# Performance work log

Measured on AMD Instinct MI355X. Metric: run time of the kernel, lower is better.

## Reference

```python
import jax, jax.numpy as jnp
import numpy as np

NUM_LAYERS = 3
N = 4096
DIM = 512
TOPK = 8
BIG = 1.0e9
EPS_COS = 1e-8
EPS_NORM = 1e-12
BN_EPS = 1e-5
LAM_K = 64.0
LAM_Z = 16.0
SIGMA_INTRA = 0.99
ALPHA = np.linspace(1.0, 1.2, NUM_LAYERS)
BETA = np.linspace(0.0, 0.0, NUM_LAYERS)


def setup_inputs() -> dict:
    key = jax.random.key(0)
    ks = jax.random.split(key, 6)
    feats = jax.random.normal(ks[0], (NUM_LAYERS, N, DIM), dtype=jnp.float32)
    labels = jax.random.randint(ks[1], (N,), 0, 64, dtype=jnp.int64)
    fc1_w = jax.random.normal(ks[2], (NUM_LAYERS, DIM, DIM), dtype=jnp.float32) * (1.0 / np.sqrt(DIM))
    fc2_w = jax.random.normal(ks[3], (NUM_LAYERS, DIM, DIM), dtype=jnp.float32) * (1.0 / np.sqrt(DIM))
    bn_gamma = jnp.ones((NUM_LAYERS, DIM), dtype=jnp.float32)
    bn_beta = jnp.zeros((NUM_LAYERS, DIM), dtype=jnp.float32)
    proj_w = jax.random.normal(ks[4], (768, DIM), dtype=jnp.float32) * (1.0 / np.sqrt(DIM))
    return {"feats": feats, "labels": labels, "fc1_w": fc1_w, "fc2_w": fc2_w,
            "bn_gamma": bn_gamma, "bn_beta": bn_beta, "proj_w": proj_w}


def _l2norm(x, axis=-1):
    return x / jnp.maximum(jnp.linalg.norm(x, axis=axis, keepdims=True), EPS_NORM)


def _pairwise_cosine(G):
    Gn = _l2norm(G)
    sim = Gn @ Gn.T
    return jnp.clip(sim, -1.0 + EPS_COS, 1.0 - EPS_COS)


def _knn_mask(sim, base_mask, topk):
    n = sim.shape[0]
    masked = (sim - BIG * jnp.eye(n, dtype=sim.dtype)) * base_mask - (1.0 - base_mask) * BIG
    k = min(topk, max(n - 1, 1))
    idx = jax.lax.top_k(masked, k)[1]  # [N, k]
    st = jnp.zeros_like(sim).at[jnp.arange(n)[:, None], idx].set(1.0)
    return jnp.maximum(st, st.T)


def _build_intra_inter(sim, labels, topk):
    same = (labels[None, :] == labels[:, None]).astype(sim.dtype)
    diff = 1.0 - same
    m_intra = _knn_mask(sim, same, topk)
    m_inter = _knn_mask(sim, diff, topk)
    sim_intra = jnp.maximum(sim * m_intra, 0.0)
    sim_inter = jnp.maximum(sim * m_inter, 0.0)
    return sim_intra, sim_inter


def _normalize_sym(sim_graph, eps=1e-8):
    d = jnp.maximum(sim_graph.sum(axis=1), eps)
    dinv = d ** -0.5
    return dinv[:, None] * sim_graph * dinv[None, :]  # == diag(dinv) @ S @ diag(dinv)


def _diffusion(K, t_diff=1):
    out = K
    for _ in range(max(t_diff - 1, 0)):
        out = out @ K
    return out


def _bn_train(x, gamma, beta):
    m = x.mean(axis=0)
    v = x.var(axis=0)  # biased, as torch BN training
    return (x - m) / jnp.sqrt(v + BN_EPS) * gamma + beta


def _gam(S, G, w1, w2, gamma, beta):
    Z = S @ (G @ w1.T)
    Z = jax.nn.relu(_bn_train(Z, gamma, beta))
    Z = S @ (Z @ w2.T)
    return Z + G


def reference(feats, labels, fc1_w, fc2_w, bn_gamma, bn_beta, proj_w):
    n = feats.shape[1]
    eye = jnp.eye(n, dtype=feats.dtype)
    same = (labels[None, :] == labels[:, None]).astype(feats.dtype)

    K_list, Z_list = [], []
    for i in range(NUM_LAYERS):
        G = feats[i]
        sim = _pairwise_cosine(G)
        sim_intra, sim_inter = _build_intra_inter(sim, labels, TOPK)
        sim_graph = float(ALPHA[i]) * sim_intra + float(BETA[i]) * sim_inter + 1e-6 * eye
        S = _normalize_sym(sim_graph)
        K = _diffusion(S, t_diff=1)
        Z = _gam(S, G, fc1_w[i], fc2_w[i], bn_gamma[i], bn_beta[i])
        K_list.append(K)
        Z_list.append(Z)

    loss_K = jnp.zeros((), dtype=feats.dtype)
    loss_Z = jnp.zeros((), dtype=feats.dtype)
    for i in range(1, NUM_LAYERS):
        K_tgt = jax.lax.stop_gradient(K_list[i])
        loss_K = loss_K + jnp.mean((K_list[i - 1] - K_tgt) ** 2)
        Zp = _l2norm(Z_list[i - 1] @ proj_w.T)
        Zc = _l2norm(Z_list[i] @ proj_w.T)
        loss_Z = loss_Z + jnp.mean((Zp - jax.lax.stop_gradient(Zc)) ** 2)

    K_idea = _diffusion(same * SIGMA_INTRA, t_diff=1)
    loss_idea = jnp.mean((K_list[-1] - K_idea) ** 2)
    return LAM_K * loss_K + LAM_Z * loss_Z + loss_idea
```

## Files before the change

kernel.cpp:

```cpp
#include <hip/hip_runtime.h>
#include <math.h>
#include <stdint.h>

#define NROWS 4096
#define DIM   512
#define NCLS  64
#define CAP   128
#define PD    768
#define NL    3

typedef __attribute__((ext_vector_type(8))) short short8v;
typedef __attribute__((ext_vector_type(4))) float f32x4;

__device__ __forceinline__ unsigned short f2bf(float f) {
  unsigned u = __float_as_uint(f);
  unsigned r = (u + 0x7FFF + ((u >> 16) & 1)) >> 16;
  return (unsigned short)r;
}

__device__ __forceinline__ void gload_lds16(const void* g, void* l) {
  auto* lp = reinterpret_cast<__attribute__((address_space(3))) unsigned int*>(
      reinterpret_cast<uintptr_t>(l));
  const auto* gp = reinterpret_cast<const __attribute__((address_space(1))) unsigned int*>(
      reinterpret_cast<uintptr_t>(g));
  __builtin_amdgcn_global_load_lds(gp, lp, 16, 0, 0);
}

__device__ __forceinline__ float waveReduce(float v) {
#pragma unroll
  for (int o = 32; o > 0; o >>= 1) v += __shfl_down(v, o);
  return v;
}

__device__ __forceinline__ float blockReduce(float v) {
  __shared__ float sh[4];
  int lane = threadIdx.x & 63, wv = threadIdx.x >> 6;
  v = waveReduce(v);
  if (lane == 0) sh[wv] = v;
  __syncthreads();
  float t = 0.f;
  if (threadIdx.x == 0) {
    int nw = (blockDim.x + 63) >> 6;
    for (int i = 0; i < nw; ++i) t += sh[i];
  }
  return t;
}

__global__ __launch_bounds__(256) void k_hist(const int* __restrict__ labels, int* __restrict__ chunkCnt) {
  __shared__ int h[NCLS];
  int t = threadIdx.x;
  if (t < NCLS) h[t] = 0;
  __syncthreads();
  atomicAdd(&h[labels[blockIdx.x * 256 + t]], 1);
  __syncthreads();
  if (t < NCLS) chunkCnt[blockIdx.x * NCLS + t] = h[t];
}

__global__ void k_scan(const int* __restrict__ chunkCnt, int* __restrict__ cnt,
                       int* __restrict__ off, int* __restrict__ chunkBase, float* __restrict__ acc) {
  __shared__ int sc[NCLS];
  int c = threadIdx.x;
  if (c < 8) acc[c] = 0.f;
  int tot = 0;
  for (int b = 0; b < 16; ++b) tot += chunkCnt[b * NCLS + c];
  cnt[c] = tot;
  sc[c] = tot;
  __syncthreads();
  if (c == 0) {
    int s = 0;
    for (int i = 0; i < NCLS; ++i) { int tv = sc[i]; sc[i] = s; s += tv; }
  }
  __syncthreads();
  int run = sc[c];
  off[c] = run;
  for (int b = 0; b < 16; ++b) { chunkBase[b * NCLS + c] = run; run += chunkCnt[b * NCLS + c]; }
  if (c == 0) off[NCLS] = NROWS;
}

__global__ __launch_bounds__(256) void k_scatter(const int* __restrict__ labels, const int* __restrict__ chunkBase,
                                                 int* __restrict__ perm, int* __restrict__ clsp) {
  __shared__ int lab[256];
  int t = threadIdx.x;
  int r = blockIdx.x * 256 + t;
  int c = labels[r];
  lab[t] = c;
  __syncthreads();
  int rank = 0;
  for (int j = 0; j < t; ++j) rank += (lab[j] == c);
  int pos = chunkBase[blockIdx.x * NCLS + c] + rank;
  perm[pos] = r;
  clsp[pos] = c;
}

__global__ __launch_bounds__(128) void k_prep(const float* __restrict__ feats, const int* __restrict__ perm,
                                              unsigned short* __restrict__ Gpb, float* __restrict__ invn) {
  __shared__ float red[2];
  int l = blockIdx.y;
  const float* G = feats + (size_t)l * NROWS * DIM;
  unsigned short* Gp = Gpb + (size_t)l * NROWS * DIM;
  int row = blockIdx.x, t = threadIdx.x;
  const float4* src = (const float4*)(G + (size_t)perm[row] * DIM);
  float4 v = src[t];
  ushort4 b;
  b.x = f2bf(v.x); b.y = f2bf(v.y); b.z = f2bf(v.z); b.w = f2bf(v.w);
  *(ushort4*)(Gp + (size_t)row * DIM + t * 4) = b;
  float ss = v.x * v.x + v.y * v.y + v.z * v.z + v.w * v.w;
  ss = waveReduce(ss);
  if ((t & 63) == 0) red[t >> 6] = ss;
  __syncthreads();
  if (t == 0) invn[l * NROWS + row] = 1.f / fmaxf(sqrtf(red[0] + red[1]), 1e-12f);
}

__global__ __launch_bounds__(256) void k_tobf16all(const float4* __restrict__ fc1, const float4* __restrict__ fc2,
                                                   const float4* __restrict__ proj,
                                                   ushort4* __restrict__ w1, ushort4* __restrict__ w2,
                                                   ushort4* __restrict__ pj) {
  const int nW = NL * DIM * DIM / 4;
  const int nP = PD * DIM / 4;
  int i = blockIdx.x * 256 + threadIdx.x;
  const float4* src; ushort4* dst; int k;
  if (i < nW) { src = fc1; dst = w1; k = i; }
  else if (i < 2 * nW) { src = fc2; dst = w2; k = i - nW; }
  else if (i < 2 * nW + nP) { src = proj; dst = pj; k = i - 2 * nW; }
  else return;
  float4 v = src[k];
  ushort4 o;
  o.x = f2bf(v.x); o.y = f2bf(v.y); o.z = f2bf(v.z); o.w = f2bf(v.w);
  dst[k] = o;
}

__global__ __launch_bounds__(256) void k_sim(const unsigned short* __restrict__ Gpb,
                                             const float* __restrict__ invn,
                                             const int* __restrict__ cnt, const int* __restrict__ off,
                                             float* __restrict__ sim) {
  int l = blockIdx.z;
  const unsigned short* Gp = Gpb + (size_t)l * NROWS * DIM;
  const float* inv = invn + (size_t)l * NROWS;
  float* sm = sim + (size_t)l * NCLS * CAP * CAP;
  int c = blockIdx.y;
  int n = min(cnt[c], CAP);
  int ti = blockIdx.x >> 2, tj = blockIdx.x & 3;
  if (ti * 32 >= n || tj * 32 >= n) return;
  int base = off[c];
  __shared__ short As[32][40];
  __shared__ short Bs[32][40];
  const int t = threadIdx.x;
  const int lane = t & 63, wv = t >> 6;
  const int qi = wv >> 1, qj = wv & 1;
  const int fr = lane & 15, kg = lane >> 4;
  const int half = t >> 7, tt = t & 127;
  const int srow = tt >> 2, scol = (tt & 3) * 8;
  int gr = (half ? tj : ti) * 32 + srow;
  const unsigned short* ps = Gp + (size_t)(base + min(gr, n - 1)) * DIM + scol;
  short* dst = half ? &Bs[srow][scol] : &As[srow][scol];
  f32x4 acc = {};
  for (int k0 = 0; k0 < DIM; k0 += 32) {
    short8v v = *(const short8v*)(ps + k0);
    __syncthreads();
    *(short8v*)dst = v;
    __syncthreads();
    short8v af = *(const short8v*)&As[qi * 16 + fr][kg * 8];
    short8v bf = *(const short8v*)&Bs[qj * 16 + fr][kg * 8];
    acc = __builtin_amdgcn_mfma_f32_16x16x32_bf16(af, bf, acc, 0, 0, 0);
  }
  int gj = tj * 32 + qj * 16 + fr;
  int r0 = ti * 32 + qi * 16 + kg * 4;
  if (gj < n) {
    float sj = inv[base + gj];
#pragma unroll
    for (int r = 0; r < 4; ++r) {
      int gi = r0 + r;
      if (gi < n) {
        float v = acc[r] * inv[base + gi] * sj;
        v = fminf(fmaxf(v, -1.0f + 1e-8f), 1.0f - 1e-8f);
        sm[((size_t)c * CAP + gi) * CAP + gj] = v;
      }
    }
  }
}

__global__ __launch_bounds__(64) void k_topk(const float* __restrict__ sim, const int* __restrict__ cnt,
                                             const int* __restrict__ off, const int* __restrict__ clsp,
                                             int* __restrict__ t8) {
  int l = blockIdx.y;
  const float* sm = sim + (size_t)l * NCLS * CAP * CAP;
  int* t8l = t8 + (size_t)l * NROWS * 8;
  int pr = blockIdx.x * 64 + threadIdx.x;
  if (pr >= NROWS) return;
  int c = clsp[pr];
  int n = min(cnt[c], CAP);
  int loc = pr - off[c];
  const float* row = sm + ((size_t)c * CAP + loc) * CAP;
  float bv[8]; int bi[8];
#pragma unroll
  for (int q = 0; q < 8; ++q) { bv[q] = -3e38f; bi[q] = -1; }
  for (int j = 0; j < n; ++j) {
    if (j == loc) continue;
    float v = row[j];
    if (v > bv[7]) {
      bv[7] = v; bi[7] = j;
#pragma unroll
      for (int q = 7; q > 0; --q) {
        if (bv[q] > bv[q - 1]) {
          float tv = bv[q]; bv[q] = bv[q - 1]; bv[q - 1] = tv;
          int tq = bi[q]; bi[q] = bi[q - 1]; bi[q - 1] = tq;
        }
      }
    }
  }
#pragma unroll
  for (int q = 0; q < 8; ++q) t8l[pr * 8 + q] = bi[q];
}

__global__ __launch_bounds__(256) void k_buildS1(const float* __restrict__ sim, const int* __restrict__ cnt,
                                                 const int* __restrict__ off, const int* __restrict__ t8,
                                                 float* __restrict__ S, float* __restrict__ dinv) {
  int l = blockIdx.z;
  float alpha = 1.0f + 0.1f * l;
  const float* sm = sim + (size_t)l * NCLS * CAP * CAP;
  float* Sl = S + (size_t)l * NCLS * CAP * CAP;
  const int* t8l = t8 + (size_t)l * NROWS * 8;
  float* dv = dinv + (size_t)l * NCLS * CAP;
  int c = blockIdx.x;
  int n = min(cnt[c], CAP);
  int i0 = blockIdx.y * 32;
  if (i0 >= n) return;
  int base = off[c];
  __shared__ int sh8[CAP * 8];
  for (int i = threadIdx.x; i < n * 8; i += 256) sh8[i] = t8l[base * 8 + i];
  __syncthreads();
  int r = threadIdx.x >> 3;
  int lj = threadIdx.x & 7;
  int i = i0 + r;
  float d = 0.f;
  if (i < n) {
    int my8[8];
#pragma unroll
    for (int q = 0; q < 8; ++q) my8[q] = sh8[i * 8 + q];
    const float* srow = sm + ((size_t)c * CAP + i) * CAP;
    float* wrow = Sl + ((size_t)c * CAP + i) * CAP;
    for (int j = lj; j < n; j += 8) {
      float w;
      if (j == i) w = 1e-6f;
      else {
        bool m = false;
#pragma unroll
        for (int q = 0; q < 8; ++q) m = m || (my8[q] == j) || (sh8[j * 8 + q] == i);
        w = m ? alpha * fmaxf(srow[j], 0.f) : 0.f;
      }
      wrow[j] = w;
      d += w;
    }
  }
  d += __shfl_xor(d, 1);
  d += __shfl_xor(d, 2);
  d += __shfl_xor(d, 4);
  if (lj == 0 && i < n) dv[c * CAP + i] = 1.f / sqrtf(fmaxf(d, 1e-8f));
}

__global__ __launch_bounds__(256) void k_buildS2(float* __restrict__ S, const float* __restrict__ dinv,
                                                 const int* __restrict__ cnt) {
  int l = blockIdx.z;
  float* Sl = S + (size_t)l * NCLS * CAP * CAP;
  const float* dv = dinv + (size_t)l * NCLS * CAP;
  int c = blockIdx.x;
  int n = min(cnt[c], CAP);
  int i0 = blockIdx.y * 32;
  if (i0 >= n) return;
  __shared__ float sd[CAP];
  for (int k = threadIdx.x; k < n; k += 256) sd[k] = dv[c * CAP + k];
  __syncthreads();
  for (int p = threadIdx.x; p < 32 * CAP; p += 256) {
    int r = p >> 7, j = p & (CAP - 1);
    int i = i0 + r;
    if (i < n && j < n)
      Sl[((size_t)c * CAP + i) * CAP + j] *= sd[i] * sd[j];
  }
}

__global__ __launch_bounds__(256) void k_gemm_bf16(const short* __restrict__ A, const short* __restrict__ B,
                                                   float* __restrict__ C, int N,
                                                   long sA, long sB, long sC) {
  int l = blockIdx.z;
  A += (size_t)l * sA; B += (size_t)l * sB; C += (size_t)l * sC;
  __shared__ __align__(16) short As[128][32];
  __shared__ __align__(16) short Bs[128][32];
  const int row0 = blockIdx.x * 128, col0 = blockIdx.y * 128;
  const int t = threadIdx.x;
  const int lane = t & 63, wv = t >> 6;
  const int wm = wv >> 1, wn = wv & 1;
  const int fr = lane & 15, kg = lane >> 4;
  const int srow = lane >> 2, skb = (lane & 3) * 8;
  const short* pa = A + (size_t)(row0 + wv * 32 + srow) * DIM + skb;
  const short* pb = B + (size_t)(col0 + wv * 32 + srow) * DIM + skb;
  f32x4 acc[4][4] = {};
  for (int kt = 0; kt < DIM; kt += 32) {
    __syncthreads();
    gload_lds16(pa + kt, &As[wv * 32][0]);
    gload_lds16(pa + kt + (size_t)16 * DIM, &As[wv * 32 + 16][0]);
    gload_lds16(pb + kt, &Bs[wv * 32][0]);
    gload_lds16(pb + kt + (size_t)16 * DIM, &Bs[wv * 32 + 16][0]);
    __syncthreads();
    short8v af[4], bf[4];
#pragma unroll
    for (int i = 0; i < 4; ++i) {
      af[i] = *(const short8v*)&As[wm * 64 + i * 16 + fr][kg * 8];
      bf[i] = *(const short8v*)&Bs[wn * 64 + i * 16 + fr][kg * 8];
    }
#pragma unroll
    for (int i = 0; i < 4; ++i)
#pragma unroll
      for (int j = 0; j < 4; ++j)
        acc[i][j] = __builtin_amdgcn_mfma_f32_16x16x32_bf16(af[i], bf[j], acc[i][j], 0, 0, 0);
  }
#pragma unroll
  for (int i = 0; i < 4; ++i) {
    int r0 = row0 + wm * 64 + i * 16 + kg * 4;
#pragma unroll
    for (int j = 0; j < 4; ++j) {
      int cc = col0 + wn * 64 + j * 16 + fr;
#pragma unroll
      for (int r = 0; r < 4; ++r)
        C[(size_t)(r0 + r) * N + cc] = acc[i][j][r];
    }
  }
}

__global__ __launch_bounds__(256) void k_spmm4(const float* __restrict__ S, const float* __restrict__ X,
                                               const float* __restrict__ Gfeat, const int* __restrict__ perm,
                                               float* __restrict__ Y, unsigned short* __restrict__ Yb,
                                               const int* __restrict__ cnt, const int* __restrict__ off) {
  int l = blockIdx.z >> 2;
  int zc = blockIdx.z & 3;
  const float* Sl = S + (size_t)l * NCLS * CAP * CAP;
  const float4* X4 = (const float4*)(X + (size_t)l * NROWS * DIM);
  const float4* G4 = Gfeat ? (const float4*)(Gfeat + (size_t)l * NROWS * DIM) : (const float4*)nullptr;
  float4* Y4 = Y ? (float4*)(Y + (size_t)l * NROWS * DIM) : (float4*)nullptr;
  ushort4* Yb4 = Yb ? (ushort4*)(Yb + (size_t)l * NROWS * DIM) : (ushort4*)nullptr;
  int c = blockIdx.x;
  int n = min(cnt[c], CAP);
  int i0 = zc * 32;
  if (i0 >= n) return;
  int base = off[c];
  int col4 = blockIdx.y * 64 + (threadIdx.x & 63);
  int ty = threadIdx.x >> 6;
  __shared__ float sS[32][CAP];
  for (int idx = threadIdx.x; idx < 32 * n; idx += 256) {
    int r = idx / n, j = idx - r * n;
    sS[r][j] = (i0 + r < n) ? Sl[((size_t)c * CAP + i0 + r) * CAP + j] : 0.f;
  }
  __syncthreads();
  float4 acc[8];
#pragma unroll
  for (int ii = 0; ii < 8; ++ii) acc[ii] = make_float4(0.f, 0.f, 0.f, 0.f);
  for (int j = 0; j < n; ++j) {
    float4 x = X4[(size_t)(base + j) * 128 + col4];
#pragma unroll
    for (int ii = 0; ii < 8; ++ii) {
      float s = sS[ty * 8 + ii][j];
      acc[ii].x += s * x.x;
      acc[ii].y += s * x.y;
      acc[ii].z += s * x.z;
      acc[ii].w += s * x.w;
    }
  }
#pragma unroll
  for (int ii = 0; ii < 8; ++ii) {
    int r = i0 + ty * 8 + ii;
    if (r < n) {
      size_t o = (size_t)(base + r) * 128 + col4;
      float4 v = acc[ii];
      if (G4) {
        float4 g = G4[(size_t)perm[base + r] * 128 + col4];
        v.x += g.x; v.y += g.y; v.z += g.z; v.w += g.w;
      }
      if (Yb4) {
        ushort4 ob;
        ob.x = f2bf(v.x); ob.y = f2bf(v.y); ob.z = f2bf(v.z); ob.w = f2bf(v.w);
        Yb4[o] = ob;
      } else {
        Y4[o] = v;
      }
    }
  }
}

#define PARTSZ (size_t)((NROWS / 32) * 1024)

__global__ __launch_bounds__(256) void k_colstats(const float* __restrict__ X, float* __restrict__ part) {
  int l = blockIdx.y;
  const float* Xl = X + (size_t)l * NROWS * DIM;
  float* pl = part + (size_t)l * PARTSZ;
  int rb = blockIdx.x, t = threadIdx.x;
#pragma unroll
  for (int cp = 0; cp < 2; ++cp) {
    int col = cp * 256 + t;
    float s = 0.f, s2 = 0.f;
    for (int r = 0; r < 32; ++r) {
      float v = Xl[(size_t)(rb * 32 + r) * DIM + col];
      s += v; s2 += v * v;
    }
    pl[rb * 1024 + col] = s;
    pl[rb * 1024 + 512 + col] = s2;
  }
}

__global__ __launch_bounds__(64) void k_bnfin(const float* __restrict__ part, const float* __restrict__ gamma,
                                              const float* __restrict__ beta, float* __restrict__ sc) {
  int l = blockIdx.y;
  const float* pl = part + (size_t)l * PARTSZ;
  int k = blockIdx.x * 64 + threadIdx.x;
  float s = 0.f, s2 = 0.f;
  for (int b = 0; b < NROWS / 32; ++b) {
    s += pl[b * 1024 + k];
    s2 += pl[b * 1024 + 512 + k];
  }
  float m = s * (1.f / NROWS);
  float var = s2 * (1.f / NROWS) - m * m;
  float sg = gamma[l * DIM + k] / sqrtf(var + 1e-5f);
  sc[l * 2 * DIM + k] = sg;
  sc[l * 2 * DIM + DIM + k] = beta[l * DIM + k] - m * sg;
}

__global__ __launch_bounds__(256) void k_bnrelu(const float4* __restrict__ X, const float* __restrict__ sc,
                                                ushort4* __restrict__ Yb) {
  int l = blockIdx.y;
  const float4* Xl = X + (size_t)l * (NROWS * DIM / 4);
  const float* scl = sc + (size_t)l * 2 * DIM;
  ushort4* Yl = Yb + (size_t)l * (NROWS * DIM / 4);
  int i = blockIdx.x * blockDim.x + threadIdx.x;
  int cb = (i * 4) & (DIM - 1);
  float4 v = Xl[i];
  ushort4 o;
  o.x = f2bf(fmaxf(v.x * scl[cb + 0] + scl[DIM + cb + 0], 0.f));
  o.y = f2bf(fmaxf(v.y * scl[cb + 1] + scl[DIM + cb + 1], 0.f));
  o.z = f2bf(fmaxf(v.z * scl[cb + 2] + scl[DIM + cb + 2], 0.f));
  o.w = f2bf(fmaxf(v.w * scl[cb + 3] + scl[DIM + cb + 3], 0.f));
  Yl[i] = o;
}

__global__ __launch_bounds__(192) void k_rownormP(float* __restrict__ P) {
  __shared__ float red[3];
  __shared__ float s_inv;
  int l = blockIdx.y;
  float* Pl = P + (size_t)l * NROWS * PD;
  int row = blockIdx.x, t = threadIdx.x;
  float4* p = (float4*)(Pl + (size_t)row * PD);
  float4 v = p[t];
  float ss = v.x * v.x + v.y * v.y + v.z * v.z + v.w * v.w;
  ss = waveReduce(ss);
  if ((t & 63) == 0) red[t >> 6] = ss;
  __syncthreads();
  if (t == 0) s_inv = 1.f / fmaxf(sqrtf(red[0] + red[1] + red[2]), 1e-12f);
  __syncthreads();
  float inv = s_inv;
  v.x *= inv; v.y *= inv; v.z *= inv; v.w *= inv;
  p[t] = v;
}

__global__ __launch_bounds__(256) void k_lossdiff(const float* __restrict__ P, int n, float coef,
                                                  float* __restrict__ acc) {
  int y = blockIdx.y;
  const float* A = P + (size_t)y * NROWS * PD;
  const float* B = A + (size_t)NROWS * PD;
  float s = 0.f;
  for (int i = blockIdx.x * blockDim.x + threadIdx.x; i < n; i += gridDim.x * blockDim.x) {
    float d = A[i] - B[i];
    s += d * d;
  }
  s = blockReduce(s);
  if (threadIdx.x == 0) atomicAdd(acc, s * coef);
}

__global__ __launch_bounds__(256) void k_lossS(const float* __restrict__ S, const int* __restrict__ cnt,
                                               float target, float cK, float cI,
                                               float* __restrict__ acc) {
  int y = blockIdx.y;
  const float* Sa = S + (size_t)y * NCLS * CAP * CAP;
  const float* Sb = nullptr;
  float coef;
  if (y < 2) { Sb = Sa + (size_t)NCLS * CAP * CAP; coef = cK; }
  else { Sa = S + (size_t)2 * NCLS * CAP * CAP; coef = cI; }
  int c = blockIdx.x;
  int n = min(cnt[c], CAP);
  float s = 0.f;
  for (int p = threadIdx.x; p < CAP * CAP; p += 256) {
    int i = p >> 7, j = p & (CAP - 1);
    if (i < n && j < n) {
      size_t o = ((size_t)c * CAP + i) * CAP + j;
      float d = Sb ? (Sa[o] - Sb[o]) : (Sa[o] - target);
      s += d * d;
    }
  }
  s = blockReduce(s);
  if (threadIdx.x == 0) atomicAdd(acc, s * coef);
}

__global__ void k_final(const float* __restrict__ acc, float* __restrict__ out) {
  if (threadIdx.x == 0) out[0] = acc[0];
}

extern "C" void kernel_launch(void* const* d_in, const int* in_sizes, int n_in,
                              void* d_out, int out_size, void* d_ws, size_t ws_size,
                              hipStream_t stream) {
  const float* feats = (const float*)d_in[0];
  const int* labels = (const int*)d_in[1];
  const float* fc1 = (const float*)d_in[2];
  const float* fc2 = (const float*)d_in[3];
  const float* gamma = (const float*)d_in[4];
  const float* beta = (const float*)d_in[5];
  const float* proj = (const float*)d_in[6];
  float* out = (float*)d_out;

  char* w = (char*)d_ws;
  auto alloc = [&](size_t bytes) { char* p = w; w += (bytes + 255) & ~(size_t)255; return p; };
  float* bufA = (float*)alloc((size_t)NL * NROWS * DIM * 4);
  float* bufB = (float*)alloc((size_t)NL * NROWS * DIM * 4);
  unsigned short* Gpb = (unsigned short*)alloc((size_t)NL * NROWS * DIM * 2);
  unsigned short* actb = (unsigned short*)alloc((size_t)NL * NROWS * DIM * 2);
  unsigned short* W1b = (unsigned short*)alloc((size_t)NL * DIM * DIM * 2);
  unsigned short* W2b = (unsigned short*)alloc((size_t)NL * DIM * DIM * 2);
  unsigned short* Pjb = (unsigned short*)alloc((size_t)PD * DIM * 2);
  float* sim  = (float*)alloc((size_t)NL * NCLS * CAP * CAP * 4);
  float* S    = (float*)alloc((size_t)NL * NCLS * CAP * CAP * 4);
  float* P    = (float*)alloc((size_t)NL * NROWS * PD * 4);
  float* invn = (float*)alloc((size_t)NL * NROWS * 4);
  float* dinv = (float*)alloc((size_t)NL * NCLS * CAP * 4);
  float* part = (float*)alloc((size_t)NL * PARTSZ * 4);
  float* bnsc = (float*)alloc((size_t)NL * 2 * DIM * 4);
  float* acc  = (float*)alloc(256);
  int* cnt  = (int*)alloc(NCLS * 4);
  int* offc = (int*)alloc((NCLS + 1) * 4);
  int* perm = (int*)alloc(NROWS * 4);
  int* clsp = (int*)alloc(NROWS * 4);
  int* t8   = (int*)alloc((size_t)NL * NROWS * 8 * 4);
  int* chunkCnt  = (int*)alloc(16 * NCLS * 4);
  int* chunkBase = (int*)alloc(16 * NCLS * 4);

  const float LAM_K = 64.f, LAM_Z = 16.f, SIGMA = 0.99f;
  const float cK = LAM_K / ((float)NROWS * (float)NROWS);
  const float cZ = LAM_Z / ((float)NROWS * (float)PD);
  const float cI = 1.f / ((float)NROWS * (float)NROWS);
  const long sAct = (long)NROWS * DIM;
  const long sW = (long)DIM * DIM;

  hipLaunchKernelGGL(k_hist, dim3(16), dim3(256), 0, stream, labels, chunkCnt);
  hipLaunchKernelGGL(k_scan, dim3(1), dim3(64), 0, stream, chunkCnt, cnt, offc, chunkBase, acc);
  hipLaunchKernelGGL(k_scatter, dim3(16), dim3(256), 0, stream, labels, chunkBase, perm, clsp);
  hipLaunchKernelGGL(k_tobf16all, dim3((2 * NL * DIM * DIM / 4 + PD * DIM / 4 + 255) / 256), dim3(256), 0, stream,
                     (const float4*)fc1, (const float4*)fc2, (const float4*)proj,
                     (ushort4*)W1b, (ushort4*)W2b, (ushort4*)Pjb);

  hipLaunchKernelGGL(k_prep, dim3(NROWS, NL), dim3(128), 0, stream, feats, perm, Gpb, invn);
  hipLaunchKernelGGL(k_sim, dim3(16, NCLS, NL), dim3(256), 0, stream, Gpb, invn, cnt, offc, sim);
  hipLaunchKernelGGL(k_topk, dim3(NROWS / 64, NL), dim3(64), 0, stream, sim, cnt, offc, clsp, t8);
  hipLaunchKernelGGL(k_buildS1, dim3(NCLS, CAP / 32, NL), dim3(256), 0, stream, sim, cnt, offc, t8, S, dinv);
  hipLaunchKernelGGL(k_buildS2, dim3(NCLS, CAP / 32, NL), dim3(256), 0, stream, S, dinv, cnt);

  hipLaunchKernelGGL(k_gemm_bf16, dim3(NROWS / 128, DIM / 128, NL), dim3(256), 0, stream,
                     (const short*)Gpb, (const short*)W1b, bufA, DIM, sAct, sW, (long)NROWS * DIM);
  hipLaunchKernelGGL(k_spmm4, dim3(NCLS, DIM / 256, 4 * NL), dim3(256), 0, stream, S, bufA,
                     (const float*)nullptr, (const int*)nullptr, bufB, (unsigned short*)nullptr, cnt, offc);
  hipLaunchKernelGGL(k_colstats, dim3(NROWS / 32, NL), dim3(256), 0, stream, bufB, part);
  hipLaunchKernelGGL(k_bnfin, dim3(DIM / 64, NL), dim3(64), 0, stream, part, gamma, beta, bnsc);
  hipLaunchKernelGGL(k_bnrelu, dim3(NROWS * DIM / 4 / 256, NL), dim3(256), 0, stream,
                     (const float4*)bufB, bnsc, (ushort4*)actb);
  hipLaunchKernelGGL(k_gemm_bf16, dim3(NROWS / 128, DIM / 128, NL), dim3(256), 0, stream,
                     (const short*)actb, (const short*)W2b, bufB, DIM, sAct, sW, (long)NROWS * DIM);
  hipLaunchKernelGGL(k_spmm4, dim3(NCLS, DIM / 256, 4 * NL), dim3(256), 0, stream, S, bufB,
                     feats, perm, (float*)nullptr, actb, cnt, offc);
  hipLaunchKernelGGL(k_gemm_bf16, dim3(NROWS / 128, PD / 128, NL), dim3(256), 0, stream,
                     (const short*)actb, (const short*)Pjb, P, PD, sAct, 0L, (long)NROWS * PD);
  hipLaunchKernelGGL(k_rownormP, dim3(NROWS, NL), dim3(192), 0, stream, P);

  hipLaunchKernelGGL(k_lossS, dim3(NCLS, 3), dim3(256), 0, stream, S, cnt, SIGMA, cK, cI, acc);
  hipLaunchKernelGGL(k_lossdiff, dim3(512, 2), dim3(256), 0, stream, P, NROWS * PD, cZ, acc);

  hipLaunchKernelGGL(k_final, dim3(1), dim3(64), 0, stream, acc, out);
}
```

Measured before the change: 281.6 us.

## Run per-class graph SpMM on bf16 MFMA and emit bf16 GEMM outputs

Replaces the fp32 FMA-based per-class S·X aggregation with a bf16 MFMA tile kernel that stages S (converted to bf16) and a transposed bf16 X tile in LDS. The preceding weight GEMMs now write bf16 directly, halving intermediate traffic. The top-k kernel is also changed to use 256-thread blocks and float4 row loads. The intent is to cut FMA-bound aggregation time and memory traffic, at the cost of extra bf16 rounding of S and of the intermediate activations, plus a non-coalesced transpose store into LDS.

```diff
diff --git a/kernel.cpp b/kernel.cpp
--- a/kernel.cpp
+++ b/kernel.cpp
@@ -179,31 +179,38 @@
   }
 }
 
-__global__ __launch_bounds__(64) void k_topk(const float* __restrict__ sim, const int* __restrict__ cnt,
-                                             const int* __restrict__ off, const int* __restrict__ clsp,
-                                             int* __restrict__ t8) {
+__global__ __launch_bounds__(256) void k_topk(const float* __restrict__ sim, const int* __restrict__ cnt,
+                                              const int* __restrict__ off, const int* __restrict__ clsp,
+                                              int* __restrict__ t8) {
   int l = blockIdx.y;
   const float* sm = sim + (size_t)l * NCLS * CAP * CAP;
   int* t8l = t8 + (size_t)l * NROWS * 8;
-  int pr = blockIdx.x * 64 + threadIdx.x;
+  int pr = blockIdx.x * 256 + threadIdx.x;
   if (pr >= NROWS) return;
   int c = clsp[pr];
   int n = min(cnt[c], CAP);
   int loc = pr - off[c];
-  const float* row = sm + ((size_t)c * CAP + loc) * CAP;
+  const float4* row4 = (const float4*)(sm + ((size_t)c * CAP + loc) * CAP);
   float bv[8]; int bi[8];
 #pragma unroll
   for (int q = 0; q < 8; ++q) { bv[q] = -3e38f; bi[q] = -1; }
-  for (int j = 0; j < n; ++j) {
-    if (j == loc) continue;
-    float v = row[j];
-    if (v > bv[7]) {
-      bv[7] = v; bi[7] = j;
-#pragma unroll
-      for (int q = 7; q > 0; --q) {
-        if (bv[q] > bv[q - 1]) {
-          float tv = bv[q]; bv[q] = bv[q - 1]; bv[q - 1] = tv;
-          int tq = bi[q]; bi[q] = bi[q - 1]; bi[q - 1] = tq;
+  for (int j4 = 0; j4 < CAP / 4; ++j4) {
+    if (j4 * 4 >= n) break;
+    float4 v4 = row4[j4];
+    float vv[4] = {v4.x, v4.y, v4.z, v4.w};
+#pragma unroll
+    for (int k = 0; k < 4; ++k) {
+      int j = j4 * 4 + k;
+      if (j >= n || j == loc) continue;
+      float v = vv[k];
+      if (v > bv[7]) {
+        bv[7] = v; bi[7] = j;
+#pragma unroll
+        for (int q = 7; q > 0; --q) {
+          if (bv[q] > bv[q - 1]) {
+            float tv = bv[q]; bv[q] = bv[q - 1]; bv[q - 1] = tv;
+            int tq = bi[q]; bi[q] = bi[q - 1]; bi[q - 1] = tq;
+          }
         }
       }
     }
@@ -279,10 +286,11 @@
 }
 
 __global__ __launch_bounds__(256) void k_gemm_bf16(const short* __restrict__ A, const short* __restrict__ B,
-                                                   float* __restrict__ C, int N,
-                                                   long sA, long sB, long sC) {
+                                                   float* __restrict__ C, unsigned short* __restrict__ Cb,
+                                                   int N, long sA, long sB, long sC) {
   int l = blockIdx.z;
-  A += (size_t)l * sA; B += (size_t)l * sB; C += (size_t)l * sC;
+  A += (size_t)l * sA; B += (size_t)l * sB;
+  if (Cb) Cb += (size_t)l * sC; else C += (size_t)l * sC;
   __shared__ __align__(16) short As[128][32];
   __shared__ __align__(16) short Bs[128][32];
   const int row0 = blockIdx.x * 128, col0 = blockIdx.y * 128;
@@ -320,66 +328,97 @@
     for (int j = 0; j < 4; ++j) {
       int cc = col0 + wn * 64 + j * 16 + fr;
 #pragma unroll
-      for (int r = 0; r < 4; ++r)
-        C[(size_t)(r0 + r) * N + cc] = acc[i][j][r];
-    }
-  }
-}
-
-__global__ __launch_bounds__(256) void k_spmm4(const float* __restrict__ S, const float* __restrict__ X,
-                                               const float* __restrict__ Gfeat, const int* __restrict__ perm,
-                                               float* __restrict__ Y, unsigned short* __restrict__ Yb,
-                                               const int* __restrict__ cnt, const int* __restrict__ off) {
-  int l = blockIdx.z >> 2;
-  int zc = blockIdx.z & 3;
+      for (int r = 0; r < 4; ++r) {
+        if (Cb) Cb[(size_t)(r0 + r) * N + cc] = f2bf(acc[i][j][r]);
+        else C[(size_t)(r0 + r) * N + cc] = acc[i][j][r];
+      }
+    }
+  }
+}
+
+__global__ __launch_bounds__(256) void k_spmm_mfma(const float* __restrict__ S, const unsigned short* __restrict__ Xb,
+                                                   const float* __restrict__ Gfeat, const int* __restrict__ perm,
+                                                   float* __restrict__ Y, unsigned short* __restrict__ Yb,
+                                                   const int* __restrict__ cnt, const int* __restrict__ off) {
+  int l = blockIdx.z;
   const float* Sl = S + (size_t)l * NCLS * CAP * CAP;
-  const float4* X4 = (const float4*)(X + (size_t)l * NROWS * DIM);
-  const float4* G4 = Gfeat ? (const float4*)(Gfeat + (size_t)l * NROWS * DIM) : (const float4*)nullptr;
-  float4* Y4 = Y ? (float4*)(Y + (size_t)l * NROWS * DIM) : (float4*)nullptr;
-  ushort4* Yb4 = Yb ? (ushort4*)(Yb + (size_t)l * NROWS * DIM) : (ushort4*)nullptr;
+  const unsigned short* Xl = Xb + (size_t)l * NROWS * DIM;
+  const float* Gl = Gfeat ? Gfeat + (size_t)l * NROWS * DIM : (const float*)nullptr;
+  float* Yl = Y ? Y + (size_t)l * NROWS * DIM : (float*)nullptr;
+  unsigned short* Ybl = Yb ? Yb + (size_t)l * NROWS * DIM : (unsigned short*)nullptr;
   int c = blockIdx.x;
   int n = min(cnt[c], CAP);
-  int i0 = zc * 32;
-  if (i0 >= n) return;
   int base = off[c];
-  int col4 = blockIdx.y * 64 + (threadIdx.x & 63);
-  int ty = threadIdx.x >> 6;
-  __shared__ float sS[32][CAP];
-  for (int idx = threadIdx.x; idx < 32 * n; idx += 256) {
-    int r = idx / n, j = idx - r * n;
-    sS[r][j] = (i0 + r < n) ? Sl[((size_t)c * CAP + i0 + r) * CAP + j] : 0.f;
-  }
-  __syncthreads();
-  float4 acc[8];
-#pragma unroll
-  for (int ii = 0; ii < 8; ++ii) acc[ii] = make_float4(0.f, 0.f, 0.f, 0.f);
-  for (int j = 0; j < n; ++j) {
-    float4 x = X4[(size_t)(base + j) * 128 + col4];
-#pragma unroll
-    for (int ii = 0; ii < 8; ++ii) {
-      float s = sS[ty * 8 + ii][j];
-      acc[ii].x += s * x.x;
-      acc[ii].y += s * x.y;
-      acc[ii].z += s * x.z;
-      acc[ii].w += s * x.w;
-    }
-  }
-#pragma unroll
-  for (int ii = 0; ii < 8; ++ii) {
-    int r = i0 + ty * 8 + ii;
-    if (r < n) {
-      size_t o = (size_t)(base + r) * 128 + col4;
-      float4 v = acc[ii];
-      if (G4) {
-        float4 g = G4[(size_t)perm[base + r] * 128 + col4];
-        v.x += g.x; v.y += g.y; v.z += g.z; v.w += g.w;
+  int d0 = blockIdx.y * 128;
+  __shared__ short As[128][40];
+  __shared__ short Bs[128][34];
+  const int t = threadIdx.x;
+  const int lane = t & 63, wv = t >> 6;
+  const int wm = wv >> 1, wn = wv & 1;
+  const int fr = lane & 15, kg = lane >> 4;
+  f32x4 acc[4][4] = {};
+  int nk = (n + 31) >> 5;
+  for (int kt = 0; kt < nk; ++kt) {
+    int j0 = kt * 32;
+    __syncthreads();
+    {
+      int ra = t >> 1, jj0 = (t & 1) * 16;
+      const float* srow = Sl + ((size_t)c * CAP + (ra < n ? ra : 0)) * CAP + j0 + jj0;
+      short tmp[16];
+#pragma unroll
+      for (int q = 0; q < 16; ++q) {
+        int j = j0 + jj0 + q;
+        float v = (ra < n && j < n) ? srow[q] : 0.f;
+        tmp[q] = (short)f2bf(v);
       }
-      if (Yb4) {
-        ushort4 ob;
-        ob.x = f2bf(v.x); ob.y = f2bf(v.y); ob.z = f2bf(v.z); ob.w = f2bf(v.w);
-        Yb4[o] = ob;
-      } else {
-        Y4[o] = v;
+      *(short8v*)&As[ra][jj0] = *(short8v*)&tmp[0];
+      *(short8v*)&As[ra][jj0 + 8] = *(short8v*)&tmp[8];
+    }
+    {
+      int pr = t >> 4, dg = t & 15;
+      int ja = j0 + 2 * pr, jb = ja + 1;
+      const unsigned short* xa = Xl + (size_t)(base + (ja < n ? ja : 0)) * DIM + d0 + dg * 8;
+      const unsigned short* xb = Xl + (size_t)(base + (jb < n ? jb : 0)) * DIM + d0 + dg * 8;
+      ushort4 a0 = ja < n ? *(const ushort4*)xa : make_ushort4(0, 0, 0, 0);
+      ushort4 a1 = ja < n ? *(const ushort4*)(xa + 4) : make_ushort4(0, 0, 0, 0);
+      ushort4 b0 = jb < n ? *(const ushort4*)xb : make_ushort4(0, 0, 0, 0);
+      ushort4 b1 = jb < n ? *(const ushort4*)(xb + 4) : make_ushort4(0, 0, 0, 0);
+      unsigned short av[8] = {a0.x, a0.y, a0.z, a0.w, a1.x, a1.y, a1.z, a1.w};
+      unsigned short bvv[8] = {b0.x, b0.y, b0.z, b0.w, b1.x, b1.y, b1.z, b1.w};
+#pragma unroll
+      for (int q = 0; q < 8; ++q) {
+        *(unsigned int*)&Bs[dg * 8 + q][2 * pr] = (unsigned int)av[q] | ((unsigned int)bvv[q] << 16);
+      }
+    }
+    __syncthreads();
+    short8v af[4], bf[4];
+#pragma unroll
+    for (int i = 0; i < 4; ++i) {
+      af[i] = *(const short8v*)&As[wm * 64 + i * 16 + fr][kg * 8];
+      bf[i] = *(const short8v*)&Bs[wn * 64 + i * 16 + fr][kg * 8];
+    }
+#pragma unroll
+    for (int i = 0; i < 4; ++i)
+#pragma unroll
+      for (int j = 0; j < 4; ++j)
+        acc[i][j] = __builtin_amdgcn_mfma_f32_16x16x32_bf16(af[i], bf[j], acc[i][j], 0, 0, 0);
+  }
+#pragma unroll
+  for (int i = 0; i < 4; ++i) {
+    int gi0 = wm * 64 + i * 16 + kg * 4;
+#pragma unroll
+    for (int j = 0; j < 4; ++j) {
+      int d = d0 + wn * 64 + j * 16 + fr;
+#pragma unroll
+      for (int r = 0; r < 4; ++r) {
+        int gi = gi0 + r;
+        if (gi < n) {
+          size_t o = (size_t)(base + gi) * DIM + d;
+          float v = acc[i][j][r];
+          if (Gl) v += Gl[(size_t)perm[base + gi] * DIM + d];
+          if (Ybl) Ybl[o] = f2bf(v);
+          else Yl[o] = v;
+        }
       }
     }
   }
@@ -514,7 +553,7 @@
 
   char* w = (char*)d_ws;
   auto alloc = [&](size_t bytes) { char* p = w; w += (bytes + 255) & ~(size_t)255; return p; };
-  float* bufA = (float*)alloc((size_t)NL * NROWS * DIM * 4);
+  unsigned short* Xib = (unsigned short*)alloc((size_t)NL * NROWS * DIM * 2);
   float* bufB = (float*)alloc((size_t)NL * NROWS * DIM * 4);
   unsigned short* Gpb = (unsigned short*)alloc((size_t)NL * NROWS * DIM * 2);
   unsigned short* actb = (unsigned short*)alloc((size_t)NL * NROWS * DIM * 2);
@@ -553,24 +592,24 @@
 
   hipLaunchKernelGGL(k_prep, dim3(NROWS, NL), dim3(128), 0, stream, feats, perm, Gpb, invn);
   hipLaunchKernelGGL(k_sim, dim3(16, NCLS, NL), dim3(256), 0, stream, Gpb, invn, cnt, offc, sim);
-  hipLaunchKernelGGL(k_topk, dim3(NROWS / 64, NL), dim3(64), 0, stream, sim, cnt, offc, clsp, t8);
+  hipLaunchKernelGGL(k_topk, dim3(NROWS / 256, NL), dim3(256), 0, stream, sim, cnt, offc, clsp, t8);
   hipLaunchKernelGGL(k_buildS1, dim3(NCLS, CAP / 32, NL), dim3(256), 0, stream, sim, cnt, offc, t8, S, dinv);
   hipLaunchKernelGGL(k_buildS2, dim3(NCLS, CAP / 32, NL), dim3(256), 0, stream, S, dinv, cnt);
 
   hipLaunchKernelGGL(k_gemm_bf16, dim3(NROWS / 128, DIM / 128, NL), dim3(256), 0, stream,
-                     (const short*)Gpb, (const short*)W1b, bufA, DIM, sAct, sW, (long)NROWS * DIM);
-  hipLaunchKernelGGL(k_spmm4, dim3(NCLS, DIM / 256, 4 * NL), dim3(256), 0, stream, S, bufA,
+                     (const short*)Gpb, (const short*)W1b, (float*)nullptr, Xib, DIM, sAct, sW, (long)NROWS * DIM);
+  hipLaunchKernelGGL(k_spmm_mfma, dim3(NCLS, DIM / 128, NL), dim3(256), 0, stream, S, Xib,
                      (const float*)nullptr, (const int*)nullptr, bufB, (unsigned short*)nullptr, cnt, offc);
   hipLaunchKernelGGL(k_colstats, dim3(NROWS / 32, NL), dim3(256), 0, stream, bufB, part);
   hipLaunchKernelGGL(k_bnfin, dim3(DIM / 64, NL), dim3(64), 0, stream, part, gamma, beta, bnsc);
   hipLaunchKernelGGL(k_bnrelu, dim3(NROWS * DIM / 4 / 256, NL), dim3(256), 0, stream,
                      (const float4*)bufB, bnsc, (ushort4*)actb);
   hipLaunchKernelGGL(k_gemm_bf16, dim3(NROWS / 128, DIM / 128, NL), dim3(256), 0, stream,
-                     (const short*)actb, (const short*)W2b, bufB, DIM, sAct, sW, (long)NROWS * DIM);
-  hipLaunchKernelGGL(k_spmm4, dim3(NCLS, DIM / 256, 4 * NL), dim3(256), 0, stream, S, bufB,
+                     (const short*)actb, (const short*)W2b, (float*)nullptr, Xib, DIM, sAct, sW, (long)NROWS * DIM);
+  hipLaunchKernelGGL(k_spmm_mfma, dim3(NCLS, DIM / 128, NL), dim3(256), 0, stream, S, Xib,
                      feats, perm, (float*)nullptr, actb, cnt, offc);
   hipLaunchKernelGGL(k_gemm_bf16, dim3(NROWS / 128, PD / 128, NL), dim3(256), 0, stream,
-                     (const short*)actb, (const short*)Pjb, P, PD, sAct, 0L, (long)NROWS * PD);
+                     (const short*)actb, (const short*)Pjb, P, (unsigned short*)nullptr, PD, sAct, 0L, (long)NROWS * PD);
   hipLaunchKernelGGL(k_rownormP, dim3(NROWS, NL), dim3(192), 0, stream, P);
 
   hipLaunchKernelGGL(k_lossS, dim3(NCLS, 3), dim3(256), 0, stream, S, cnt, SIGMA, cK, cI, acc);
```

Measured after the change: 295.0 us. +4.8%, slower.
